# Optimization experiments

Measured on AMD Instinct MI355X. Metric: run time of the kernel, lower is better.

Reference implementation:

```python
import jax, jax.numpy as jnp
import numpy as np

D_MODEL, D_STATE, D_CONV = 1024, 16, 4
B, L = 2, 2048


def setup_inputs() -> dict:
    key = jax.random.key(0)
    ks = jax.random.split(key, 12)
    d, n, k = D_MODEL, D_STATE, D_CONV
    s = lambda fan_in: 1.0 / np.sqrt(fan_in)
    inp = {
        "x": jax.random.normal(ks[0], (B, L, d), dtype=jnp.float32),
        # Linear weights stored as (in, out): y = x @ W + b
        "W_in": jax.random.uniform(ks[1], (d, 2 * d), minval=-s(d), maxval=s(d)),
        "b_in": jax.random.uniform(ks[2], (2 * d,), minval=-s(d), maxval=s(d)),
        # depthwise conv: (out_ch=d, in_ch/groups=1, kernel=k)
        "W_conv": jax.random.uniform(ks[3], (d, 1, k), minval=-s(k), maxval=s(k)),
        "b_conv": jax.random.uniform(ks[4], (d,), minval=-s(k), maxval=s(k)),
        "W_xp": jax.random.uniform(ks[5], (d, 3 * n), minval=-s(d), maxval=s(d)),
        "b_xp": jax.random.uniform(ks[6], (3 * n,), minval=-s(d), maxval=s(d)),
        "W_dt": jax.random.uniform(ks[7], (n, d), minval=-s(n), maxval=s(n)),
        "b_dt": jax.random.uniform(ks[8], (d,), minval=-s(n), maxval=s(n)),
        # A param initialized as in torch: arange(1, n+1) tiled over d rows
        "A_log": jnp.tile(jnp.arange(1, n + 1, dtype=jnp.float32), (d, 1)),
        "W_out": jax.random.uniform(ks[9], (d, d), minval=-s(d), maxval=s(d)),
        "b_out": jax.random.uniform(ks[10], (d,), minval=-s(d), maxval=s(d)),
    }
    return inp


def _forward(x, W_in, b_in, W_conv, b_conv, W_xp, b_xp, W_dt, b_dt, A_log, W_out, b_out):
    n = D_STATE
    k = W_conv.shape[-1]
    silu = jax.nn.silu

    xz = x @ W_in + b_in                       # (B, L, 2d)
    u, z = jnp.split(xz, 2, axis=-1)

    # causal depthwise conv1d: torch pads k-1 both sides then keeps first L
    uc = jnp.transpose(u, (0, 2, 1))           # (B, d, L)
    uc = jax.lax.conv_general_dilated(
        uc, W_conv, window_strides=(1,), padding=[(k - 1, 0)],
        dimension_numbers=("NCH", "OIH", "NCH"), feature_group_count=D_MODEL,
    ) + b_conv[None, :, None]
    u = silu(jnp.transpose(uc, (0, 2, 1)))     # (B, L, d)

    x_db = u @ W_xp + b_xp                     # (B, L, 3n)
    dt_in, Bm, Cm = jnp.split(x_db, [n, 2 * n], axis=-1)
    dt = jax.nn.softplus(dt_in @ W_dt + b_dt)  # (B, L, d)

    A = -jnp.exp(A_log)                        # (d, n)
    dA = jnp.exp(jnp.einsum("bld,dn->bldn", dt, A))          # (B, L, d, n)
    dBu = (dt * u)[..., None] * Bm[:, :, None, :]              # (B, L, d, n)

    def step(h, inputs):
        dA_t, dBu_t, C_t = inputs              # (B,d,n), (B,d,n), (B,n)
        h = dA_t * h + dBu_t
        y = jnp.einsum("bdn,bn->bd", h, C_t)
        return h, y

    h0 = jnp.zeros((x.shape[0], D_MODEL, n), dtype=x.dtype)
    xs = (jnp.transpose(dA, (1, 0, 2, 3)),
          jnp.transpose(dBu, (1, 0, 2, 3)),
          jnp.transpose(Cm, (1, 0, 2)))
    _, ys = jax.lax.scan(step, h0, xs)         # (L, B, d)
    y = jnp.transpose(ys, (1, 0, 2))           # (B, L, d)

    y = y * silu(z)
    return y @ W_out + b_out


def reference(x, W_in, b_in, W_conv, b_conv, W_xp, b_xp, W_dt, b_dt, A_log, W_out, b_out):
    return _forward(x, W_in, b_in, W_conv, b_conv, W_xp, b_xp, W_dt, b_dt, A_log, W_out, b_out)
```

## Files before the change

kernel.cpp:

```cpp
#include <hip/hip_runtime.h>
#include <math.h>

#define D_MODEL 1024
#define D_STATE 16
#define BATCH   2
#define SEQ     2048
#define M_ROWS  (BATCH*SEQ)
#define KP      3072
#define CH      32
#define NCHUNK  (SEQ/CH)

typedef unsigned short ushortT;
typedef ushortT ushortx4 __attribute__((ext_vector_type(4)));
typedef ushortT ushortx8 __attribute__((ext_vector_type(8)));
typedef short   shortx8  __attribute__((ext_vector_type(8)));
typedef float   f32x4    __attribute__((ext_vector_type(4)));

__device__ __forceinline__ float silu_f(float x) {
    return x / (1.0f + __expf(-x));
}
__device__ __forceinline__ ushortT f2bf_rne(float f) {
    unsigned u = __float_as_uint(f);
    u += 0x7FFF + ((u >> 16) & 1);
    return (ushortT)(u >> 16);
}
__device__ __forceinline__ float bf2f(ushortT h) {
    return __uint_as_float(((unsigned)h) << 16);
}

__global__ __launch_bounds__(256)
void split_x_kernel(const float* __restrict__ X, ushortT* __restrict__ Xs)
{
    int gid = blockIdx.x * 256 + threadIdx.x;
    const int KQ = D_MODEL / 4;
    if (gid >= M_ROWS * KQ) return;
    int row = gid / KQ, kc = gid % KQ;
    float4 v = *reinterpret_cast<const float4*>(X + (size_t)row * D_MODEL + kc * 4);
    float vv[4] = {v.x, v.y, v.z, v.w};
    ushortx4 h, l;
#pragma unroll
    for (int i = 0; i < 4; ++i) {
        ushortT hi = f2bf_rne(vv[i]);
        h[i] = hi;
        l[i] = f2bf_rne(vv[i] - bf2f(hi));
    }
    ushortT* base = Xs + (size_t)row * KP + kc * 4;
    *(ushortx4*)(base)              = h;
    *(ushortx4*)(base + D_MODEL)     = l;
    *(ushortx4*)(base + 2 * D_MODEL) = h;
}

__global__ __launch_bounds__(256)
void wsplit_t_kernel(const float* __restrict__ W, ushortT* __restrict__ Wt, int N)
{
    __shared__ float tile[32][33];
    const int K = D_MODEL;
    int nb = blockIdx.x * 32, kb = blockIdx.y * 32;
    int tx = threadIdx.x & 31;
    int ty = threadIdx.x >> 5;
#pragma unroll
    for (int i = 0; i < 4; ++i) {
        int k = ty + i * 8;
        tile[k][tx] = W[(size_t)(kb + k) * N + nb + tx];
    }
    __syncthreads();
#pragma unroll
    for (int i = 0; i < 4; ++i) {
        int n = ty + i * 8;
        float v = tile[tx][n];
        ushortT hi = f2bf_rne(v);
        ushortT lo = f2bf_rne(v - bf2f(hi));
        ushortT* base = Wt + (size_t)(nb + n) * KP + kb + tx;
        base[0]     = hi;
        base[K]     = hi;
        base[2 * K] = lo;
    }
}

__global__ __launch_bounds__(256)
void wsplit_xp_kernel(const float* __restrict__ W, ushortT* __restrict__ Wt)
{
    int gid = blockIdx.x * 256 + threadIdx.x;
    if (gid >= 64 * D_MODEL) return;
    int k = gid & (D_MODEL - 1);
    int n = gid >> 10;
    ushortT hi = 0, lo = 0;
    if (n < 48) {
        float v = W[(size_t)k * 48 + n];
        hi = f2bf_rne(v);
        lo = f2bf_rne(v - bf2f(hi));
    }
    ushortT* base = Wt + (size_t)n * KP + k;
    base[0]           = hi;
    base[D_MODEL]     = hi;
    base[2 * D_MODEL] = lo;
}

__global__ __launch_bounds__(256)
void gemm_mfma_split(const ushortT* __restrict__ A,
                     const ushortT* __restrict__ Bt,
                     const float* __restrict__ bias,
                     float* __restrict__ C0,
                     float* __restrict__ C1,
                     int N, int split)
{
    __shared__ char lds[32768];
    char* Asm = lds;
    char* Bsm = lds + 16384;

    const int tid  = threadIdx.x;
    const int lane = tid & 63;
    const int wid  = tid >> 6;
    const int wr   = wid >> 1;
    const int wc   = wid & 1;

    const int nwg  = gridDim.x * gridDim.y;
    const int wgid = blockIdx.y * gridDim.x + blockIdx.x;
    const int qc   = nwg >> 3;
    const int swz  = (wgid & 7) * qc + (wgid >> 3);
    const int bx   = swz % gridDim.x;
    const int by   = swz / gridDim.x;
    const int brow = by * 128;
    const int bcol = bx * 128;

    f32x4 acc[4][4];
#pragma unroll
    for (int i = 0; i < 4; ++i)
#pragma unroll
        for (int j = 0; j < 4; ++j) {
            acc[i][j][0] = 0.f; acc[i][j][1] = 0.f;
            acc[i][j][2] = 0.f; acc[i][j][3] = 0.f;
        }

    const ushortT* Ag = A  + (size_t)brow * KP;
    const ushortT* Bg = Bt + (size_t)bcol * KP;

    ushortx8 ra0[4], rb0[4], ra1[4], rb1[4];

#define SLOAD(ra, rb, k0)                                                      \
    {                                                                          \
        _Pragma("unroll")                                                      \
        for (int q = 0; q < 4; ++q) {                                          \
            int slot = tid + q * 256;                                          \
            int row = slot >> 3, kc = slot & 7;                                \
            ra[q] = *(const ushortx8*)(Ag + (size_t)row * KP + (k0) + kc * 8); \
            rb[q] = *(const ushortx8*)(Bg + (size_t)row * KP + (k0) + kc * 8); \
        }                                                                      \
    }

#define SWRITE(ra, rb)                                                         \
    {                                                                          \
        _Pragma("unroll")                                                      \
        for (int q = 0; q < 4; ++q) {                                          \
            int slot = tid + q * 256;                                          \
            int row = slot >> 3, kc = slot & 7;                                \
            int byt = row * 128 + ((kc * 16) ^ ((row & 7) << 4));              \
            *(ushortx8*)(Asm + byt) = ra[q];                                   \
            *(ushortx8*)(Bsm + byt) = rb[q];                                   \
        }                                                                      \
    }

#define COMPUTE()                                                              \
    {                                                                          \
        _Pragma("unroll")                                                      \
        for (int ks = 0; ks < 2; ++ks) {                                       \
            shortx8 af[4], bfr[4];                                             \
            _Pragma("unroll")                                                  \
            for (int mt = 0; mt < 4; ++mt) {                                   \
                int row = wr * 64 + mt * 16 + (lane & 15);                     \
                int kc = ks * 4 + (lane >> 4);                                 \
                int byt = row * 128 + ((kc * 16) ^ ((row & 7) << 4));          \
                af[mt] = *(const shortx8*)(Asm + byt);                         \
            }                                                                  \
            _Pragma("unroll")                                                  \
            for (int nt = 0; nt < 4; ++nt) {                                   \
                int row = wc * 64 + nt * 16 + (lane & 15);                     \
                int kc = ks * 4 + (lane >> 4);                                 \
                int byt = row * 128 + ((kc * 16) ^ ((row & 7) << 4));          \
                bfr[nt] = *(const shortx8*)(Bsm + byt);                        \
            }                                                                  \
            _Pragma("unroll")                                                  \
            for (int mt = 0; mt < 4; ++mt)                                     \
                _Pragma("unroll")                                              \
                for (int nt = 0; nt < 4; ++nt)                                 \
                    acc[mt][nt] = __builtin_amdgcn_mfma_f32_16x16x32_bf16(     \
                        af[mt], bfr[nt], acc[mt][nt], 0, 0, 0);                \
        }                                                                      \
    }

    SLOAD(ra0, rb0, 0);
    const int NS = KP / 64;
    for (int s = 0; s < NS; s += 2) {
        __syncthreads();
        SWRITE(ra0, rb0);
        __syncthreads();
        if (s + 1 < NS) SLOAD(ra1, rb1, (s + 1) * 64);
        COMPUTE();
        __syncthreads();
        SWRITE(ra1, rb1);
        __syncthreads();
        if (s + 2 < NS) SLOAD(ra0, rb0, (s + 2) * 64);
        COMPUTE();
    }

#undef SLOAD
#undef SWRITE
#undef COMPUTE

    const bool inC0  = (bcol < split);
    float* dst       = inC0 ? C0 : C1;
    const int ldc    = inC0 ? split : (N - split);
    const int cb     = bcol - (inC0 ? 0 : split);

#pragma unroll
    for (int mt = 0; mt < 4; ++mt)
#pragma unroll
        for (int nt = 0; nt < 4; ++nt)
#pragma unroll
            for (int j = 0; j < 4; ++j) {
                int r  = brow + wr * 64 + mt * 16 + (lane >> 4) * 4 + j;
                int cg = wc * 64 + nt * 16 + (lane & 15);
                dst[(size_t)r * ldc + cb + cg] = acc[mt][nt][j] + bias[bcol + cg];
            }
}

__global__ __launch_bounds__(256)
void gemm_xp_mfma(const ushortT* __restrict__ A,
                  const ushortT* __restrict__ Bt,
                  float* __restrict__ Part)
{
    __shared__ char lds[24576];
    char* Asm = lds;
    char* Bsm = lds + 16384;

    const int tid  = threadIdx.x;
    const int lane = tid & 63;
    const int wid  = tid >> 6;
    const int ksp  = blockIdx.x;
    const int brow = blockIdx.y * 128;
    const int kbase = ksp * (KP / 4);

    f32x4 acc[2][4];
#pragma unroll
    for (int i = 0; i < 2; ++i)
#pragma unroll
        for (int j = 0; j < 4; ++j) {
            acc[i][j][0] = 0.f; acc[i][j][1] = 0.f;
            acc[i][j][2] = 0.f; acc[i][j][3] = 0.f;
        }

    const ushortT* Ag = A  + (size_t)brow * KP + kbase;
    const ushortT* Bg = Bt + kbase;

    for (int s = 0; s < 12; ++s) {
        const int k0 = s * 64;
        ushortx8 ra[4], rb[2];
#pragma unroll
        for (int q = 0; q < 4; ++q) {
            int slot = tid + q * 256;
            int row = slot >> 3, kc = slot & 7;
            ra[q] = *(const ushortx8*)(Ag + (size_t)row * KP + k0 + kc * 8);
        }
#pragma unroll
        for (int q = 0; q < 2; ++q) {
            int slot = tid + q * 256;
            int row = slot >> 3, kc = slot & 7;
            rb[q] = *(const ushortx8*)(Bg + (size_t)row * KP + k0 + kc * 8);
        }
        __syncthreads();
#pragma unroll
        for (int q = 0; q < 4; ++q) {
            int slot = tid + q * 256;
            int row = slot >> 3, kc = slot & 7;
            int byt = row * 128 + ((kc * 16) ^ ((row & 7) << 4));
            *(ushortx8*)(Asm + byt) = ra[q];
        }
#pragma unroll
        for (int q = 0; q < 2; ++q) {
            int slot = tid + q * 256;
            int row = slot >> 3, kc = slot & 7;
            int byt = row * 128 + ((kc * 16) ^ ((row & 7) << 4));
            *(ushortx8*)(Bsm + byt) = rb[q];
        }
        __syncthreads();
#pragma unroll
        for (int ks = 0; ks < 2; ++ks) {
            shortx8 af[2], bfr[4];
#pragma unroll
            for (int mt = 0; mt < 2; ++mt) {
                int row = wid * 32 + mt * 16 + (lane & 15);
                int kc = ks * 4 + (lane >> 4);
                int byt = row * 128 + ((kc * 16) ^ ((row & 7) << 4));
                af[mt] = *(const shortx8*)(Asm + byt);
            }
#pragma unroll
            for (int nt = 0; nt < 4; ++nt) {
                int row = nt * 16 + (lane & 15);
                int kc = ks * 4 + (lane >> 4);
                int byt = row * 128 + ((kc * 16) ^ ((row & 7) << 4));
                bfr[nt] = *(const shortx8*)(Bsm + byt);
            }
#pragma unroll
            for (int mt = 0; mt < 2; ++mt)
#pragma unroll
                for (int nt = 0; nt < 4; ++nt)
                    acc[mt][nt] = __builtin_amdgcn_mfma_f32_16x16x32_bf16(
                        af[mt], bfr[nt], acc[mt][nt], 0, 0, 0);
        }
        __syncthreads();
    }

    float* dst = Part + (size_t)ksp * M_ROWS * 64;
#pragma unroll
    for (int mt = 0; mt < 2; ++mt)
#pragma unroll
        for (int nt = 0; nt < 4; ++nt)
#pragma unroll
            for (int j = 0; j < 4; ++j) {
                int r  = brow + wid * 32 + mt * 16 + (lane >> 4) * 4 + j;
                int cg = nt * 16 + (lane & 15);
                dst[(size_t)r * 64 + cg] = acc[mt][nt][j];
            }
}

__global__ __launch_bounds__(256)
void xp_combine_kernel(const float* __restrict__ Part,
                       const float* __restrict__ b_xp,
                       float* __restrict__ x_db)
{
    int gid = blockIdx.x * 256 + threadIdx.x;
    if (gid >= M_ROWS * 12) return;
    int row = gid / 12, q = gid % 12;
    float4 a = *reinterpret_cast<const float4*>(b_xp + q * 4);
#pragma unroll
    for (int s = 0; s < 4; ++s) {
        float4 p = *reinterpret_cast<const float4*>(
            Part + ((size_t)s * M_ROWS + row) * 64 + q * 4);
        a.x += p.x; a.y += p.y; a.z += p.z; a.w += p.w;
    }
    *reinterpret_cast<float4*>(x_db + (size_t)row * 48 + q * 4) = a;
}

__global__ __launch_bounds__(256)
void conv_silu_split_kernel(const float* __restrict__ u_raw,
                            const float* __restrict__ W_conv,
                            const float* __restrict__ b_conv,
                            ushortT* __restrict__ Us)
{
    int gid = blockIdx.x * 256 + threadIdx.x;
    if (gid >= M_ROWS * D_MODEL) return;
    int c = gid % D_MODEL;
    int t = (gid / D_MODEL) % SEQ;
    int b = gid / (D_MODEL * SEQ);

    float w0 = W_conv[c * 4 + 0], w1 = W_conv[c * 4 + 1];
    float w2 = W_conv[c * 4 + 2], w3 = W_conv[c * 4 + 3];
    const float* base = u_raw + (size_t)b * SEQ * D_MODEL + c;

    float acc = b_conv[c];
    if (t >= 3) acc = fmaf(base[(size_t)(t - 3) * D_MODEL], w0, acc);
    if (t >= 2) acc = fmaf(base[(size_t)(t - 2) * D_MODEL], w1, acc);
    if (t >= 1) acc = fmaf(base[(size_t)(t - 1) * D_MODEL], w2, acc);
    acc = fmaf(base[(size_t)t * D_MODEL], w3, acc);

    float v = silu_f(acc);

    ushortT hi = f2bf_rne(v);
    ushortT lo = f2bf_rne(v - bf2f(hi));
    size_t row = (size_t)(gid / D_MODEL);
    ushortT* ub = Us + row * KP + c;
    ub[0]           = hi;
    ub[D_MODEL]     = lo;
    ub[2 * D_MODEL] = hi;
}

__global__ __launch_bounds__(256)
void scan_chunk_local(const ushortT* __restrict__ Us,
                      const float* __restrict__ x_db,
                      const float* __restrict__ A_log,
                      const float* __restrict__ W_dt,
                      const float* __restrict__ b_dt,
                      float* __restrict__ Pbuf,
                      float* __restrict__ Hloc)
{
    int gid = blockIdx.x * 256 + threadIdx.x;
    if (gid >= BATCH * NCHUNK * D_MODEL) return;
    int c     = gid % D_MODEL;
    int rem   = gid / D_MODEL;
    int chunk = rem % NCHUNK;
    int b     = rem / NCHUNK;

    float a[16], h[16], wdt[16];
#pragma unroll
    for (int i = 0; i < 16; ++i) {
        a[i]   = -__expf(A_log[c * 16 + i]);
        h[i]   = 0.f;
        wdt[i] = W_dt[i * D_MODEL + c];
    }
    const float bdt = b_dt[c];

    float dtsum = 0.f;
    size_t row = (size_t)b * SEQ + (size_t)chunk * CH;
    for (int t = 0; t < CH; ++t, ++row) {
        const float* xb = x_db + row * 48;
        float acc = bdt;
#pragma unroll
        for (int i = 0; i < 16; ++i)
            acc = fmaf(xb[i], wdt[i], acc);
        float dtv = fmaxf(acc, 0.0f) + log1pf(expf(-fabsf(acc)));

        float uv = bf2f(Us[row * KP + c]) + bf2f(Us[row * KP + D_MODEL + c]);
        float du = dtv * uv;
        dtsum += dtv;
#pragma unroll
        for (int i = 0; i < 16; ++i) {
            float dA = __expf(dtv * a[i]);
            h[i] = fmaf(dA, h[i], du * xb[16 + i]);
        }
    }

    size_t obase = ((size_t)(b * NCHUNK + chunk) * 16) * D_MODEL + c;
#pragma unroll
    for (int i = 0; i < 16; ++i) {
        Pbuf[obase + (size_t)i * D_MODEL] = __expf(a[i] * dtsum);
        Hloc[obase + (size_t)i * D_MODEL] = h[i];
    }
}

__global__ __launch_bounds__(256)
void scan_combine(const float* __restrict__ Pbuf,
                  const float* __restrict__ Hloc,
                  float* __restrict__ Hin)
{
    int gid = blockIdx.x * 256 + threadIdx.x;
    if (gid >= BATCH * 16 * D_MODEL) return;
    int c   = gid % D_MODEL;
    int rem = gid / D_MODEL;
    int i   = rem % 16;
    int b   = rem / 16;

    const size_t stride = (size_t)16 * D_MODEL;
    size_t idx = ((size_t)(b * NCHUNK) * 16 + i) * D_MODEL + c;

    float h  = 0.f;
    float Pn = Pbuf[idx];
    float Hn = Hloc[idx];
    for (int ch = 0; ch < NCHUNK; ++ch) {
        float Pc = Pn, Hc = Hn;
        if (ch + 1 < NCHUNK) {
            Pn = Pbuf[idx + stride];
            Hn = Hloc[idx + stride];
        }
        Hin[idx] = h;
        h = fmaf(Pc, h, Hc);
        idx += stride;
    }
}

__global__ __launch_bounds__(256)
void scan_chunk_final(const ushortT* __restrict__ Us,
                      const float* __restrict__ x_db,
                      const float* __restrict__ A_log,
                      const float* __restrict__ W_dt,
                      const float* __restrict__ b_dt,
                      const float* __restrict__ Hin,
                      const float* __restrict__ z,
                      ushortT* __restrict__ Ys)
{
    int gid = blockIdx.x * 256 + threadIdx.x;
    if (gid >= BATCH * NCHUNK * D_MODEL) return;
    int c     = gid % D_MODEL;
    int rem   = gid / D_MODEL;
    int chunk = rem % NCHUNK;
    int b     = rem / NCHUNK;

    size_t ibase = ((size_t)(b * NCHUNK + chunk) * 16) * D_MODEL + c;

    float a[16], h[16], wdt[16];
#pragma unroll
    for (int i = 0; i < 16; ++i) {
        a[i]   = -__expf(A_log[c * 16 + i]);
        h[i]   = Hin[ibase + (size_t)i * D_MODEL];
        wdt[i] = W_dt[i * D_MODEL + c];
    }
    const float bdt = b_dt[c];

    size_t row = (size_t)b * SEQ + (size_t)chunk * CH;
    for (int t = 0; t < CH; ++t, ++row) {
        const float* xb = x_db + row * 48;
        float acc = bdt;
#pragma unroll
        for (int i = 0; i < 16; ++i)
            acc = fmaf(xb[i], wdt[i], acc);
        float dtv = fmaxf(acc, 0.0f) + log1pf(expf(-fabsf(acc)));

        float uv = bf2f(Us[row * KP + c]) + bf2f(Us[row * KP + D_MODEL + c]);
        float du = dtv * uv;
        float yv = 0.f;
#pragma unroll
        for (int i = 0; i < 16; ++i) {
            float dA = __expf(dtv * a[i]);
            h[i] = fmaf(dA, h[i], du * xb[16 + i]);
            yv   = fmaf(h[i], xb[32 + i], yv);
        }

        float g = yv * silu_f(z[row * D_MODEL + c]);
        ushortT hi = f2bf_rne(g);
        ushortT lo = f2bf_rne(g - bf2f(hi));
        ushortT* yb = Ys + row * KP + c;
        yb[0]           = hi;
        yb[D_MODEL]     = lo;
        yb[2 * D_MODEL] = hi;
    }
}

extern "C" void kernel_launch(void* const* d_in, const int* in_sizes, int n_in,
                              void* d_out, int out_size, void* d_ws, size_t ws_size,
                              hipStream_t stream)
{
    const float* x      = (const float*)d_in[0];
    const float* W_in   = (const float*)d_in[1];
    const float* b_in   = (const float*)d_in[2];
    const float* W_conv = (const float*)d_in[3];
    const float* b_conv = (const float*)d_in[4];
    const float* W_xp   = (const float*)d_in[5];
    const float* b_xp   = (const float*)d_in[6];
    const float* W_dt   = (const float*)d_in[7];
    const float* b_dt   = (const float*)d_in[8];
    const float* A_log  = (const float*)d_in[9];
    const float* W_out  = (const float*)d_in[10];
    const float* b_out  = (const float*)d_in[11];
    float* out = (float*)d_out;

    float* ws = (float*)d_ws;
    const size_t S  = (size_t)M_ROWS * D_MODEL;
    const size_t SC = (size_t)BATCH * NCHUNK * 16 * D_MODEL;
    float* u_raw  = ws;
    float* z      = ws + S;
    float* x_db   = ws + 4 * S;
    float* Pbuf   = ws + 4 * S + 196608;
    float* HlocB  = Pbuf + SC;
    float* HinB   = HlocB + SC;
    ushortT* xs   = (ushortT*)(HinB + SC);
    ushortT* wt   = xs + (size_t)M_ROWS * KP;
    ushortT* wxp  = wt + (size_t)2048 * KP;
    float*   part = (float*)(wxp + (size_t)64 * KP);

    dim3 blk(256);

    wsplit_t_kernel<<<dim3(2 * D_MODEL / 32, D_MODEL / 32), blk, 0, stream>>>(W_in, wt, 2 * D_MODEL);
    split_x_kernel<<<dim3(M_ROWS * (D_MODEL / 4) / 256), blk, 0, stream>>>(x, xs);

    gemm_mfma_split<<<dim3(2 * D_MODEL / 128, M_ROWS / 128), blk, 0, stream>>>(
        xs, wt, b_in, u_raw, z, 2 * D_MODEL, D_MODEL);

    conv_silu_split_kernel<<<dim3(M_ROWS * D_MODEL / 256), blk, 0, stream>>>(
        u_raw, W_conv, b_conv, xs);

    wsplit_xp_kernel<<<dim3(64 * D_MODEL / 256), blk, 0, stream>>>(W_xp, wxp);
    gemm_xp_mfma<<<dim3(4, M_ROWS / 128), blk, 0, stream>>>(xs, wxp, part);
    xp_combine_kernel<<<dim3(M_ROWS * 12 / 256), blk, 0, stream>>>(part, b_xp, x_db);

    scan_chunk_local<<<dim3(BATCH * NCHUNK * D_MODEL / 256), blk, 0, stream>>>(
        xs, x_db, A_log, W_dt, b_dt, Pbuf, HlocB);
    scan_combine<<<dim3(BATCH * 16 * D_MODEL / 256), blk, 0, stream>>>(Pbuf, HlocB, HinB);

    wsplit_t_kernel<<<dim3(D_MODEL / 32, D_MODEL / 32), blk, 0, stream>>>(W_out, wt, D_MODEL);

    scan_chunk_final<<<dim3(BATCH * NCHUNK * D_MODEL / 256), blk, 0, stream>>>(
        xs, x_db, A_log, W_dt, b_dt, HinB, z, xs);

    gemm_mfma_split<<<dim3(D_MODEL / 128, M_ROWS / 128), blk, 0, stream>>>(
        xs, wt, b_out, out, out, D_MODEL, D_MODEL);
}
```

Before: 253.4 us.

## Use direct global-to-LDS loads with double buffering and split-K for output GEMM

The MFMA GEMM now stages tiles straight from global memory into LDS with global_load_lds. It uses two LDS buffers, so the next tile loads while the current one is computed, and each step needs one barrier instead of four. It replaces the register-staged load and write path. The output projection GEMM, which has only 256 tiles, is split along K into two partial results that a new combine kernel sums with the bias, giving more workgroups. In exchange, LDS use doubles to 64KB, which can lower occupancy, and the split-K path adds an extra pass over the partial buffers in memory.

```diff
diff --git a/kernel.cpp b/kernel.cpp
--- a/kernel.cpp
+++ b/kernel.cpp
@@ -26,6 +26,11 @@
 }
 __device__ __forceinline__ float bf2f(ushortT h) {
     return __uint_as_float(((unsigned)h) << 16);
+}
+__device__ __forceinline__ void gload_lds16(const void* g, void* l) {
+    __builtin_amdgcn_global_load_lds(
+        (const __attribute__((address_space(1))) void*)g,
+        (__attribute__((address_space(3))) void*)l, 16, 0, 0);
 }
 
 __global__ __launch_bounds__(256)
@@ -102,11 +107,9 @@
                      const float* __restrict__ bias,
                      float* __restrict__ C0,
                      float* __restrict__ C1,
-                     int N, int split)
-{
-    __shared__ char lds[32768];
-    char* Asm = lds;
-    char* Bsm = lds + 16384;
+                     int N, int split, int NS)
+{
+    __shared__ char lds[65536];
 
     const int tid  = threadIdx.x;
     const int lane = tid & 63;
@@ -122,6 +125,7 @@
     const int by   = swz / gridDim.x;
     const int brow = by * 128;
     const int bcol = bx * 128;
+    const int kbeg = blockIdx.z * NS * 64;
 
     f32x4 acc[4][4];
 #pragma unroll
@@ -132,36 +136,33 @@
             acc[i][j][2] = 0.f; acc[i][j][3] = 0.f;
         }
 
-    const ushortT* Ag = A  + (size_t)brow * KP;
-    const ushortT* Bg = Bt + (size_t)bcol * KP;
-
-    ushortx8 ra0[4], rb0[4], ra1[4], rb1[4];
-
-#define SLOAD(ra, rb, k0)                                                      \
+    const ushortT* Ag = A  + (size_t)brow * KP + kbeg;
+    const ushortT* Bg = Bt + (size_t)bcol * KP + kbeg;
+
+    int off[4], lslot[4];
+#pragma unroll
+    for (int q = 0; q < 4; ++q) {
+        int slot = q * 256 + tid;
+        int row = slot >> 3, kc = slot & 7;
+        off[q]   = row * KP + ((kc ^ (row & 7)) << 3);
+        lslot[q] = (q * 256 + wid * 64) * 16;
+    }
+
+#define STAGE(buf, k0)                                                         \
     {                                                                          \
+        char* Ad = lds + (buf) * 32768;                                        \
+        char* Bd = Ad + 16384;                                                 \
         _Pragma("unroll")                                                      \
         for (int q = 0; q < 4; ++q) {                                          \
-            int slot = tid + q * 256;                                          \
-            int row = slot >> 3, kc = slot & 7;                                \
-            ra[q] = *(const ushortx8*)(Ag + (size_t)row * KP + (k0) + kc * 8); \
-            rb[q] = *(const ushortx8*)(Bg + (size_t)row * KP + (k0) + kc * 8); \
+            gload_lds16(Ag + off[q] + (k0), Ad + lslot[q]);                    \
+            gload_lds16(Bg + off[q] + (k0), Bd + lslot[q]);                    \
         }                                                                      \
     }
 
-#define SWRITE(ra, rb)                                                         \
+#define COMPUTE(buf)                                                           \
     {                                                                          \
-        _Pragma("unroll")                                                      \
-        for (int q = 0; q < 4; ++q) {                                          \
-            int slot = tid + q * 256;                                          \
-            int row = slot >> 3, kc = slot & 7;                                \
-            int byt = row * 128 + ((kc * 16) ^ ((row & 7) << 4));              \
-            *(ushortx8*)(Asm + byt) = ra[q];                                   \
-            *(ushortx8*)(Bsm + byt) = rb[q];                                   \
-        }                                                                      \
-    }
-
-#define COMPUTE()                                                              \
-    {                                                                          \
+        char* Asm = lds + (buf) * 32768;                                       \
+        char* Bsm = Asm + 16384;                                               \
         _Pragma("unroll")                                                      \
         for (int ks = 0; ks < 2; ++ks) {                                       \
             shortx8 af[4], bfr[4];                                             \
@@ -188,40 +189,64 @@
         }                                                                      \
     }
 
-    SLOAD(ra0, rb0, 0);
-    const int NS = KP / 64;
-    for (int s = 0; s < NS; s += 2) {
+    STAGE(0, 0);
+    __syncthreads();
+    for (int s = 0; s < NS; ++s) {
+        const int cur = s & 1;
+        if (s + 1 < NS) STAGE(cur ^ 1, (s + 1) * 64);
+        COMPUTE(cur);
         __syncthreads();
-        SWRITE(ra0, rb0);
-        __syncthreads();
-        if (s + 1 < NS) SLOAD(ra1, rb1, (s + 1) * 64);
-        COMPUTE();
-        __syncthreads();
-        SWRITE(ra1, rb1);
-        __syncthreads();
-        if (s + 2 < NS) SLOAD(ra0, rb0, (s + 2) * 64);
-        COMPUTE();
-    }
-
-#undef SLOAD
-#undef SWRITE
+    }
+
+#undef STAGE
 #undef COMPUTE
 
-    const bool inC0  = (bcol < split);
-    float* dst       = inC0 ? C0 : C1;
-    const int ldc    = inC0 ? split : (N - split);
-    const int cb     = bcol - (inC0 ? 0 : split);
-
-#pragma unroll
-    for (int mt = 0; mt < 4; ++mt)
-#pragma unroll
-        for (int nt = 0; nt < 4; ++nt)
-#pragma unroll
-            for (int j = 0; j < 4; ++j) {
-                int r  = brow + wr * 64 + mt * 16 + (lane >> 4) * 4 + j;
-                int cg = wc * 64 + nt * 16 + (lane & 15);
-                dst[(size_t)r * ldc + cb + cg] = acc[mt][nt][j] + bias[bcol + cg];
-            }
+    if (gridDim.z == 1) {
+        const bool inC0  = (bcol < split);
+        float* dst       = inC0 ? C0 : C1;
+        const int ldc    = inC0 ? split : (N - split);
+        const int cb     = bcol - (inC0 ? 0 : split);
+#pragma unroll
+        for (int mt = 0; mt < 4; ++mt)
+#pragma unroll
+            for (int nt = 0; nt < 4; ++nt)
+#pragma unroll
+                for (int j = 0; j < 4; ++j) {
+                    int r  = brow + wr * 64 + mt * 16 + (lane >> 4) * 4 + j;
+                    int cg = wc * 64 + nt * 16 + (lane & 15);
+                    dst[(size_t)r * ldc + cb + cg] = acc[mt][nt][j] + bias[bcol + cg];
+                }
+    } else {
+        float* dst = C0 + (size_t)blockIdx.z * ((size_t)M_ROWS * N);
+#pragma unroll
+        for (int mt = 0; mt < 4; ++mt)
+#pragma unroll
+            for (int nt = 0; nt < 4; ++nt)
+#pragma unroll
+                for (int j = 0; j < 4; ++j) {
+                    int r  = brow + wr * 64 + mt * 16 + (lane >> 4) * 4 + j;
+                    int cg = wc * 64 + nt * 16 + (lane & 15);
+                    dst[(size_t)r * N + bcol + cg] = acc[mt][nt][j];
+                }
+    }
+}
+
+__global__ __launch_bounds__(256)
+void out_combine_kernel(const float* __restrict__ part,
+                        const float* __restrict__ bias,
+                        float* __restrict__ out)
+{
+    int gid = blockIdx.x * 256 + threadIdx.x;
+    if (gid >= M_ROWS * 256) return;
+    int row = gid >> 8, q = gid & 255;
+    size_t i = (size_t)row * D_MODEL + q * 4;
+    float4 b  = *reinterpret_cast<const float4*>(bias + q * 4);
+    float4 p0 = *reinterpret_cast<const float4*>(part + i);
+    float4 p1 = *reinterpret_cast<const float4*>(part + (size_t)M_ROWS * D_MODEL + i);
+    float4 r;
+    r.x = b.x + p0.x + p1.x; r.y = b.y + p0.y + p1.y;
+    r.z = b.z + p0.z + p1.z; r.w = b.w + p0.w + p1.w;
+    *reinterpret_cast<float4*>(out + i) = r;
 }
 
 __global__ __launch_bounds__(256)
@@ -537,6 +562,7 @@
     const size_t SC = (size_t)BATCH * NCHUNK * 16 * D_MODEL;
     float* u_raw  = ws;
     float* z      = ws + S;
+    float* kpart  = ws + 2 * S;
     float* x_db   = ws + 4 * S;
     float* Pbuf   = ws + 4 * S + 196608;
     float* HlocB  = Pbuf + SC;
@@ -551,8 +577,8 @@
     wsplit_t_kernel<<<dim3(2 * D_MODEL / 32, D_MODEL / 32), blk, 0, stream>>>(W_in, wt, 2 * D_MODEL);
     split_x_kernel<<<dim3(M_ROWS * (D_MODEL / 4) / 256), blk, 0, stream>>>(x, xs);
 
-    gemm_mfma_split<<<dim3(2 * D_MODEL / 128, M_ROWS / 128), blk, 0, stream>>>(
-        xs, wt, b_in, u_raw, z, 2 * D_MODEL, D_MODEL);
+    gemm_mfma_split<<<dim3(2 * D_MODEL / 128, M_ROWS / 128, 1), blk, 0, stream>>>(
+        xs, wt, b_in, u_raw, z, 2 * D_MODEL, D_MODEL, KP / 64);
 
     conv_silu_split_kernel<<<dim3(M_ROWS * D_MODEL / 256), blk, 0, stream>>>(
         u_raw, W_conv, b_conv, xs);
@@ -570,6 +596,7 @@
     scan_chunk_final<<<dim3(BATCH * NCHUNK * D_MODEL / 256), blk, 0, stream>>>(
         xs, x_db, A_log, W_dt, b_dt, HinB, z, xs);
 
-    gemm_mfma_split<<<dim3(D_MODEL / 128, M_ROWS / 128), blk, 0, stream>>>(
-        xs, wt, b_out, out, out, D_MODEL, D_MODEL);
-}
+    gemm_mfma_split<<<dim3(D_MODEL / 128, M_ROWS / 128, 2), blk, 0, stream>>>(
+        xs, wt, b_out, kpart, kpart, D_MODEL, D_MODEL, KP / 128);
+    out_combine_kernel<<<dim3(M_ROWS), blk, 0, stream>>>(kpart, b_out, out);
+}
```

Result: faster. 240.2 us (-5.2%).
